# Performance work log

Hardware: AMD Instinct MI355X
Metric: run time of the kernel (lower is better)

Reference implementation:

```python
import jax, jax.numpy as jnp
import numpy as np

B, S, V, E, H = 256, 141, 1000, 256, 512


def setup_inputs() -> dict:
    key = jax.random.key(0)
    ks = jax.random.split(key, 12)
    sd = 0.05
    return {
        "encoder_output": jax.random.normal(ks[0], (B, E), dtype=jnp.float32),
        "target_sequence": jax.random.randint(ks[1], (B, S), 0, V),
        "embedding": jax.random.normal(ks[2], (V, E), dtype=jnp.float32) * sd,
        "W_ih": jax.random.normal(ks[3], (4 * H, 2 * E), dtype=jnp.float32) * sd,
        "W_hh": jax.random.normal(ks[4], (4 * H, H), dtype=jnp.float32) * sd,
        "b_ih": jnp.zeros((4 * H,), dtype=jnp.float32),
        "b_hh": jnp.zeros((4 * H,), dtype=jnp.float32),
        "attn_W": jax.random.normal(ks[5], (H, H + E), dtype=jnp.float32) * sd,
        "attn_b": jnp.zeros((H,), dtype=jnp.float32),
        "v_w": jax.random.normal(ks[6], (H,), dtype=jnp.float32) * sd,
        "out_W": jax.random.normal(ks[7], (V, H), dtype=jnp.float32) * sd,
        "out_b": jnp.zeros((V,), dtype=jnp.float32),
    }


def reference(encoder_output, target_sequence, embedding, W_ih, W_hh, b_ih, b_hh,
              attn_W, attn_b, v_w, out_W, out_b):
    # embedded: [B, S, E] -> scan over time: [S, B, E]
    embedded = embedding[target_sequence]
    xs = jnp.swapaxes(embedded, 0, 1)

    h0 = jnp.zeros((B, H), dtype=encoder_output.dtype)
    c0 = jnp.zeros((B, H), dtype=encoder_output.dtype)

    def step(carry, x_t):
        h, c = carry  # [B, H]
        # Bahdanau attention over src_len=1 (encoder_output.unsqueeze(1))
        cat = jnp.concatenate([h, encoder_output], axis=-1)      # [B, H+E]
        energy = jnp.tanh(cat @ attn_W.T + attn_b)               # [B, H]
        score = energy @ v_w                                      # [B]
        # softmax over a single source position -> weight 1
        w = jax.nn.softmax(score[:, None], axis=1)               # [B, 1]
        context = w * encoder_output                              # [B, E]
        lstm_in = jnp.concatenate([x_t, context], axis=-1)       # [B, 2E]
        gates = lstm_in @ W_ih.T + b_ih + h @ W_hh.T + b_hh      # [B, 4H]
        i, f, g, o = jnp.split(gates, 4, axis=-1)                # torch gate order
        i = jax.nn.sigmoid(i)
        f = jax.nn.sigmoid(f)
        g = jnp.tanh(g)
        o = jax.nn.sigmoid(o)
        c_new = f * c + i * g
        h_new = o * jnp.tanh(c_new)
        return (h_new, c_new), h_new

    _, hs = jax.lax.scan(step, (h0, c0), xs)                     # hs: [S, B, H]
    logits = jnp.einsum('sbh,vh->bsv', hs, out_W) + out_b        # [B, S, V]
    return logits
```

## Files before the change

kernel.cpp:

```cpp
#include <hip/hip_runtime.h>

typedef __attribute__((ext_vector_type(8))) short bf16x8;
typedef __attribute__((ext_vector_type(4))) float f32x4;
typedef __attribute__((ext_vector_type(4))) unsigned short u16x4;

#define Bdim 256
#define Sdim 141
#define Vdim 1000
#define Edim 256
#define Hdim 512
#define G4H  2048

__device__ __forceinline__ float bf2f(unsigned short u) {
    union { unsigned int i; float f; } x; x.i = ((unsigned int)u) << 16; return x.f;
}
__device__ __forceinline__ unsigned short f2bf(float f) {
    union { float f; unsigned int i; } x; x.f = f;
    unsigned int i = x.i;
    return (unsigned short)((i + 0x7FFFu + ((i >> 16) & 1u)) >> 16);
}
__device__ __forceinline__ float sigmoid_f(float x) { return 1.f / (1.f + __expf(-x)); }
__device__ __forceinline__ float tanh_f(float x)    { return 1.f - 2.f / (__expf(2.f * x) + 1.f); }

__device__ __forceinline__ bf16x8 cvt8(const float* p) {
    const float4 v0 = ((const float4*)p)[0];
    const float4 v1 = ((const float4*)p)[1];
    bf16x8 r;
    r[0] = (short)f2bf(v0.x); r[1] = (short)f2bf(v0.y);
    r[2] = (short)f2bf(v0.z); r[3] = (short)f2bf(v0.w);
    r[4] = (short)f2bf(v1.x); r[5] = (short)f2bf(v1.y);
    r[6] = (short)f2bf(v1.z); r[7] = (short)f2bf(v1.w);
    return r;
}

__global__ __launch_bounds__(256) void f32_to_bf16_4(
    const float4* __restrict__ src, u16x4* __restrict__ dst, int n4)
{
    const int i = blockIdx.x * 256 + threadIdx.x;
    if (i < n4) {
        const float4 v = src[i];
        u16x4 r;
        r[0] = f2bf(v.x); r[1] = f2bf(v.y); r[2] = f2bf(v.z); r[3] = f2bf(v.w);
        dst[i] = r;
    }
}

template <bool BF16OUT>
__global__ __launch_bounds__(256) void gemm_bt_f32in(
    const float* __restrict__ A, int lda, int M,
    const float* __restrict__ Bw, int ldb,
    void* __restrict__ Cv, int ldc,
    const float* __restrict__ bias0,
    const float* __restrict__ bias1,
    int K)
{
    const int m0 = blockIdx.x * 128;
    const int n0 = blockIdx.y * 64;
    const int w    = threadIdx.x >> 6;
    const int l    = threadIdx.x & 63;
    const int lr   = l & 15;
    const int quad = l >> 4;

    int ra0 = m0 + w * 32 + lr;
    int ra1 = ra0 + 16;
    ra0 = ra0 < M ? ra0 : M - 1;
    ra1 = ra1 < M ? ra1 : M - 1;
    const float* pa0 = A + (size_t)ra0 * lda + quad * 8;
    const float* pa1 = A + (size_t)ra1 * lda + quad * 8;
    const float* pb[4];
#pragma unroll
    for (int nj = 0; nj < 4; ++nj)
        pb[nj] = Bw + (size_t)(n0 + nj * 16 + lr) * ldb + quad * 8;

    f32x4 acc[2][4];
#pragma unroll
    for (int mi = 0; mi < 2; ++mi)
#pragma unroll
        for (int nj = 0; nj < 4; ++nj)
            acc[mi][nj] = (f32x4){0.f, 0.f, 0.f, 0.f};

    for (int k = 0; k < K; k += 32) {
        bf16x8 a0 = cvt8(pa0 + k);
        bf16x8 a1 = cvt8(pa1 + k);
#pragma unroll
        for (int nj = 0; nj < 4; ++nj) {
            bf16x8 bb = cvt8(pb[nj] + k);
            acc[0][nj] = __builtin_amdgcn_mfma_f32_16x16x32_bf16(a0, bb, acc[0][nj], 0, 0, 0);
            acc[1][nj] = __builtin_amdgcn_mfma_f32_16x16x32_bf16(a1, bb, acc[1][nj], 0, 0, 0);
        }
    }

#pragma unroll
    for (int nj = 0; nj < 4; ++nj) {
        const int col = n0 + nj * 16 + lr;
        float bv = 0.f;
        if (bias0) bv += bias0[col];
        if (bias1) bv += bias1[col];
#pragma unroll
        for (int mi = 0; mi < 2; ++mi) {
            const int row = m0 + w * 32 + mi * 16 + quad * 4;
#pragma unroll
            for (int r = 0; r < 4; ++r) {
                if (row + r < M) {
                    const float v = acc[mi][nj][r] + bv;
                    if (BF16OUT)
                        ((unsigned short*)Cv)[(size_t)(row + r) * ldc + col] = f2bf(v);
                    else
                        ((float*)Cv)[(size_t)(row + r) * ldc + col] = v;
                }
            }
        }
    }
}

__device__ __forceinline__ void sync_agent(unsigned* bar, int bi, unsigned target) {
    __syncthreads();
    if (threadIdx.x == 0) {
        unsigned* ctr = bar + 256 + bi * 32;
        const unsigned goal = target * 32u;
        __hip_atomic_fetch_add(ctr, 1u, __ATOMIC_RELAXED, __HIP_MEMORY_SCOPE_AGENT);
        int guard = 0;
        while ((__hip_atomic_fetch_add(ctr, 0x10000u, __ATOMIC_RELAXED,
                                       __HIP_MEMORY_SCOPE_AGENT) & 0xFFFFu) < goal
               && ++guard < (1 << 16))
            __builtin_amdgcn_s_sleep(1);
        __builtin_amdgcn_fence(__ATOMIC_ACQUIRE, "workgroup");
    }
    __syncthreads();
}

__device__ __forceinline__ void sync_fast(unsigned* bar, int bi, unsigned target) {
    __syncthreads();
    if (threadIdx.x == 0) {
        unsigned* ctr = bar + 768 + bi * 32;
        const unsigned goal = target * 32u;
        __hip_atomic_fetch_add(ctr, 1u, __ATOMIC_RELAXED, __HIP_MEMORY_SCOPE_WORKGROUP);
        int guard = 0;
        while ((__hip_atomic_fetch_add(ctr, 0x10000u, __ATOMIC_RELAXED,
                                       __HIP_MEMORY_SCOPE_WORKGROUP) & 0xFFFFu) < goal
               && ++guard < (1 << 16))
            __builtin_amdgcn_s_sleep(1);
        __builtin_amdgcn_fence(__ATOMIC_ACQUIRE, "workgroup");
    }
    __syncthreads();
}

__global__ __launch_bounds__(256) void lstm_scan(
    const unsigned short* __restrict__ Whh,
    const unsigned short* __restrict__ emb_proj,
    const float* __restrict__ enc_proj,
    const int* __restrict__ tgt,
    unsigned short* __restrict__ hs,
    unsigned* __restrict__ bar)
{
    const int blk = blockIdx.x;
    const int bi  = blk & 7;
    const int ht  = blk >> 3;
    const int r0  = bi * 32;
    const int h0  = ht * 16;
    const int tid = threadIdx.x;
    const int nf   = tid >> 6;
    const int l    = tid & 63;
    const int lr   = l & 15;
    const int quad = l >> 4;

    __shared__ unsigned short w_lds[4096 * 8];
    __shared__ float g_lds[32][67];

    for (int u = tid; u < 4096; u += 256) {
        const int ulr = u & 15;
        const int uq  = (u >> 4) & 3;
        const int uk  = (u >> 6) & 15;
        const int ug  = u >> 10;
        *(bf16x8*)&w_lds[u * 8] =
            *(const bf16x8*)(Whh + (size_t)(ug * Hdim + h0 + ulr) * Hdim + uk * 32 + uq * 8);
    }

    int xcc;
    asm volatile("s_getreg_b32 %0, hwreg(HW_REG_XCC_ID)" : "=s"(xcc));
    if (tid == 0) {
        __hip_atomic_fetch_or(bar + 512 + bi * 32, 1u << (xcc & 7),
                              __ATOMIC_RELAXED, __HIP_MEMORY_SCOPE_AGENT);
        asm volatile("s_waitcnt vmcnt(0)" ::: "memory");
    }
    sync_agent(bar, bi, 1u);
    const unsigned fl = __hip_atomic_load(bar + 512 + bi * 32,
                              __ATOMIC_RELAXED, __HIP_MEMORY_SCOPE_AGENT);
    const bool fast = (fl & (fl - 1u)) == 0u;

    const int prow = tid & 31;
    const int phc  = (tid >> 5) * 2;
    const int brow = r0 + prow;

    const int* tokp = tgt + (size_t)brow * Sdim;

    const float* encp = enc_proj + (size_t)brow * G4H + h0 + phc;
    float2 env[4];
#pragma unroll
    for (int g = 0; g < 4; ++g)
        env[g] = *(const float2*)(encp + g * Hdim);

    unsigned epk[4];
    {
        const unsigned short* embp = emb_proj + (size_t)tokp[0] * G4H + h0 + phc;
#pragma unroll
        for (int g = 0; g < 4; ++g)
            epk[g] = *(const unsigned*)(embp + g * Hdim);
    }

    const size_t arow0 = (size_t)(r0 + lr) * Hdim + quad * 8;
    const size_t arow1 = (size_t)(r0 + 16 + lr) * Hdim + quad * 8;
    const unsigned short* wlp = w_lds + (size_t)nf * 1024 * 8;

    float c0 = 0.f, c1 = 0.f;

    for (int t = 0; t < Sdim; ++t) {
        const int tn = tokp[t + 1 < Sdim ? t + 1 : t];
        unsigned epkn[4];
        {
            const unsigned short* embn = emb_proj + (size_t)tn * G4H + h0 + phc;
#pragma unroll
            for (int g = 0; g < 4; ++g)
                epkn[g] = *(const unsigned*)(embn + g * Hdim);
        }

        f32x4 acc0 = (f32x4){0.f, 0.f, 0.f, 0.f};
        f32x4 acc1 = (f32x4){0.f, 0.f, 0.f, 0.f};
        if (t > 0) {
            const unsigned short* hprev = hs + (size_t)(t - 1) * (Bdim * Hdim);
#pragma unroll
            for (int k16 = 0; k16 < 16; ++k16) {
                bf16x8 a0 = *(const bf16x8*)(hprev + arow0 + k16 * 32);
                bf16x8 a1 = *(const bf16x8*)(hprev + arow1 + k16 * 32);
                bf16x8 bb = *(const bf16x8*)&wlp[(k16 * 64 + l) * 8];
                acc0 = __builtin_amdgcn_mfma_f32_16x16x32_bf16(a0, bb, acc0, 0, 0, 0);
                acc1 = __builtin_amdgcn_mfma_f32_16x16x32_bf16(a1, bb, acc1, 0, 0, 0);
            }
        }
#pragma unroll
        for (int r = 0; r < 4; ++r) {
            g_lds[quad * 4 + r][nf * 16 + lr]      = acc0[r];
            g_lds[16 + quad * 4 + r][nf * 16 + lr] = acc1[r];
        }
        __syncthreads();

        unsigned hpack = 0;
#pragma unroll
        for (int e = 0; e < 2; ++e) {
            const int c = phc + e;
            const float iv = g_lds[prow][c]      + bf2f((unsigned short)(epk[0] >> (16 * e))) + (e ? env[0].y : env[0].x);
            const float fv = g_lds[prow][16 + c] + bf2f((unsigned short)(epk[1] >> (16 * e))) + (e ? env[1].y : env[1].x);
            const float gv = g_lds[prow][32 + c] + bf2f((unsigned short)(epk[2] >> (16 * e))) + (e ? env[2].y : env[2].x);
            const float ov = g_lds[prow][48 + c] + bf2f((unsigned short)(epk[3] >> (16 * e))) + (e ? env[3].y : env[3].x);
            float cc = e ? c1 : c0;
            const float cn = sigmoid_f(fv) * cc + sigmoid_f(iv) * tanh_f(gv);
            if (e) c1 = cn; else c0 = cn;
            hpack |= ((unsigned)f2bf(sigmoid_f(ov) * tanh_f(cn))) << (16 * e);
        }
        unsigned* hsp = (unsigned*)(hs + (size_t)t * (Bdim * Hdim) + (size_t)brow * Hdim + h0 + phc);
        if (fast)
            *hsp = hpack;
        else
            __hip_atomic_store(hsp, hpack, __ATOMIC_RELAXED, __HIP_MEMORY_SCOPE_AGENT);

        if (t != Sdim - 1) {
            if (fast) sync_fast(bar, bi, (unsigned)(t + 1));
            else      sync_agent(bar, bi, (unsigned)(t + 2));
        }

#pragma unroll
        for (int g = 0; g < 4; ++g)
            epk[g] = epkn[g];
    }
}

__global__ __launch_bounds__(256) void gemm_logits(
    const unsigned short* __restrict__ A,
    const unsigned short* __restrict__ W,
    const float* __restrict__ bias,
    float* __restrict__ out)
{
    const int m0 = blockIdx.x * 128;
    const int n0 = blockIdx.y * 64;
    const int w    = threadIdx.x >> 6;
    const int l    = threadIdx.x & 63;
    const int lr   = l & 15;
    const int quad = l >> 4;

    const unsigned short* pa0 = A + (size_t)(m0 + w * 32 + lr) * Hdim + quad * 8;
    const unsigned short* pa1 = pa0 + (size_t)16 * Hdim;
    const unsigned short* pb[4];
#pragma unroll
    for (int nj = 0; nj < 4; ++nj) {
        int rb = n0 + nj * 16 + lr;
        rb = rb < Vdim ? rb : Vdim - 1;
        pb[nj] = W + (size_t)rb * Hdim + quad * 8;
    }

    f32x4 acc[2][4];
#pragma unroll
    for (int mi = 0; mi < 2; ++mi)
#pragma unroll
        for (int nj = 0; nj < 4; ++nj)
            acc[mi][nj] = (f32x4){0.f, 0.f, 0.f, 0.f};

    for (int k = 0; k < Hdim; k += 32) {
        bf16x8 a0 = *(const bf16x8*)(pa0 + k);
        bf16x8 a1 = *(const bf16x8*)(pa1 + k);
#pragma unroll
        for (int nj = 0; nj < 4; ++nj) {
            bf16x8 bb = *(const bf16x8*)(pb[nj] + k);
            acc[0][nj] = __builtin_amdgcn_mfma_f32_16x16x32_bf16(a0, bb, acc[0][nj], 0, 0, 0);
            acc[1][nj] = __builtin_amdgcn_mfma_f32_16x16x32_bf16(a1, bb, acc[1][nj], 0, 0, 0);
        }
    }

#pragma unroll
    for (int nj = 0; nj < 4; ++nj) {
        const int col = n0 + nj * 16 + lr;
        if (col >= Vdim) continue;
        const float bv = bias[col];
#pragma unroll
        for (int mi = 0; mi < 2; ++mi) {
            const int rowb = m0 + w * 32 + mi * 16 + quad * 4;
#pragma unroll
            for (int r = 0; r < 4; ++r) {
                const int row = rowb + r;
                const int s = row >> 8;
                const int b = row & 255;
                out[((size_t)b * Sdim + s) * Vdim + col] = acc[mi][nj][r] + bv;
            }
        }
    }
}

extern "C" void kernel_launch(void* const* d_in, const int* in_sizes, int n_in,
                              void* d_out, int out_size, void* d_ws, size_t ws_size,
                              hipStream_t stream) {
    const float* enc   = (const float*)d_in[0];
    const int*   tgt   = (const int*)d_in[1];
    const float* emb   = (const float*)d_in[2];
    const float* W_ih  = (const float*)d_in[3];
    const float* W_hh  = (const float*)d_in[4];
    const float* b_ih  = (const float*)d_in[5];
    const float* b_hh  = (const float*)d_in[6];
    const float* out_W = (const float*)d_in[10];
    const float* out_b = (const float*)d_in[11];
    float* out = (float*)d_out;

    char* ws = (char*)d_ws;
    unsigned short* whh_bf   = (unsigned short*)ws;
    unsigned short* outw_bf  = (unsigned short*)(ws + 2097152);
    unsigned short* emb_proj = (unsigned short*)(ws + 3121152);
    float*          enc_proj = (float*)(ws + 7217152);
    unsigned short* hs       = (unsigned short*)(ws + 9314304);
    unsigned*       bar      = (unsigned*)(ws + 46276608);

    hipMemsetAsync(bar, 0, 4096, stream);

    f32_to_bf16_4<<<dim3((262144 + 255) / 256), 256, 0, stream>>>(
        (const float4*)W_hh, (u16x4*)whh_bf, 262144);
    f32_to_bf16_4<<<dim3((128000 + 255) / 256), 256, 0, stream>>>(
        (const float4*)out_W, (u16x4*)outw_bf, 128000);

    gemm_bt_f32in<true><<<dim3(8, 32), 256, 0, stream>>>(
        emb, Edim, Vdim, W_ih, 2 * Edim, emb_proj, G4H, nullptr, nullptr, Edim);
    gemm_bt_f32in<false><<<dim3(2, 32), 256, 0, stream>>>(
        enc, Edim, Bdim, W_ih + Edim, 2 * Edim, enc_proj, G4H, b_ih, b_hh, Edim);
    lstm_scan<<<dim3(256), 256, 0, stream>>>(whh_bf, emb_proj, enc_proj, tgt, hs, bar);
    gemm_logits<<<dim3(282, 16), 256, 0, stream>>>(hs, outw_bf, out_b, out);
}
```

Before: 1.424 ms.

## Repartition LSTM scan into 16 batch groups of 16 rows with 512-thread blocks

The persistent LSTM scan now splits work into 16 batch groups of 16 rows, each spread over 16 blocks covering 32 hidden units, instead of 8 groups of 32 rows over 32 blocks of 16 hidden units. Blocks grow to 512 threads (8 waves), each wave doing one MFMA chain, so the W_hh slice kept in LDS doubles to 128 KB. Fewer blocks share each barrier, which is meant to cut the per-step grid-sync latency that dominates the sequential scan. The cost is a larger LDS footprint, scalar 16-bit h stores in place of packed pairs, and a changed barrier and flag layout.

```diff
diff --git a/kernel.cpp b/kernel.cpp
--- a/kernel.cpp
+++ b/kernel.cpp
@@ -116,8 +116,8 @@
 __device__ __forceinline__ void sync_agent(unsigned* bar, int bi, unsigned target) {
     __syncthreads();
     if (threadIdx.x == 0) {
-        unsigned* ctr = bar + 256 + bi * 32;
-        const unsigned goal = target * 32u;
+        unsigned* ctr = bar + bi * 32;
+        const unsigned goal = target * 16u;
         __hip_atomic_fetch_add(ctr, 1u, __ATOMIC_RELAXED, __HIP_MEMORY_SCOPE_AGENT);
         int guard = 0;
         while ((__hip_atomic_fetch_add(ctr, 0x10000u, __ATOMIC_RELAXED,
@@ -132,8 +132,8 @@
 __device__ __forceinline__ void sync_fast(unsigned* bar, int bi, unsigned target) {
     __syncthreads();
     if (threadIdx.x == 0) {
-        unsigned* ctr = bar + 768 + bi * 32;
-        const unsigned goal = target * 32u;
+        unsigned* ctr = bar + 512 + bi * 32;
+        const unsigned goal = target * 16u;
         __hip_atomic_fetch_add(ctr, 1u, __ATOMIC_RELAXED, __HIP_MEMORY_SCOPE_WORKGROUP);
         int guard = 0;
         while ((__hip_atomic_fetch_add(ctr, 0x10000u, __ATOMIC_RELAXED,
@@ -145,7 +145,7 @@
     __syncthreads();
 }
 
-__global__ __launch_bounds__(256) void lstm_scan(
+__global__ __launch_bounds__(512) void lstm_scan(
     const unsigned short* __restrict__ Whh,
     const unsigned short* __restrict__ emb_proj,
     const float* __restrict__ enc_proj,
@@ -154,114 +154,104 @@
     unsigned* __restrict__ bar)
 {
     const int blk = blockIdx.x;
-    const int bi  = blk & 7;
-    const int ht  = blk >> 3;
-    const int r0  = bi * 32;
-    const int h0  = ht * 16;
+    const int bi  = (blk & 7) * 2 + ((blk >> 3) & 1);
+    const int ht  = blk >> 4;
+    const int r0  = bi * 16;
+    const int h0  = ht * 32;
     const int tid = threadIdx.x;
-    const int nf   = tid >> 6;
+    const int w    = tid >> 6;
     const int l    = tid & 63;
     const int lr   = l & 15;
     const int quad = l >> 4;
 
-    __shared__ unsigned short w_lds[4096 * 8];
-    __shared__ float g_lds[32][67];
-
-    for (int u = tid; u < 4096; u += 256) {
+    __shared__ unsigned short w_lds[8192 * 8];
+    __shared__ float g_lds[16][132];
+
+    for (int u = tid; u < 8192; u += 512) {
         const int ulr = u & 15;
         const int uq  = (u >> 4) & 3;
         const int uk  = (u >> 6) & 15;
-        const int ug  = u >> 10;
+        const int us  = u >> 10;
+        const int grow = (us >> 1) * Hdim + h0 + (us & 1) * 16 + ulr;
         *(bf16x8*)&w_lds[u * 8] =
-            *(const bf16x8*)(Whh + (size_t)(ug * Hdim + h0 + ulr) * Hdim + uk * 32 + uq * 8);
+            *(const bf16x8*)(Whh + (size_t)grow * Hdim + uk * 32 + uq * 8);
     }
 
     int xcc;
     asm volatile("s_getreg_b32 %0, hwreg(HW_REG_XCC_ID)" : "=s"(xcc));
     if (tid == 0) {
-        __hip_atomic_fetch_or(bar + 512 + bi * 32, 1u << (xcc & 7),
+        __hip_atomic_fetch_or(bar + bi * 32 + 16, 1u << (xcc & 7),
                               __ATOMIC_RELAXED, __HIP_MEMORY_SCOPE_AGENT);
         asm volatile("s_waitcnt vmcnt(0)" ::: "memory");
     }
     sync_agent(bar, bi, 1u);
-    const unsigned fl = __hip_atomic_load(bar + 512 + bi * 32,
+    const unsigned fl = __hip_atomic_load(bar + bi * 32 + 16,
                               __ATOMIC_RELAXED, __HIP_MEMORY_SCOPE_AGENT);
     const bool fast = (fl & (fl - 1u)) == 0u;
 
-    const int prow = tid & 31;
-    const int phc  = (tid >> 5) * 2;
+    const int prow = tid >> 5;
+    const int phc  = tid & 31;
     const int brow = r0 + prow;
 
     const int* tokp = tgt + (size_t)brow * Sdim;
 
     const float* encp = enc_proj + (size_t)brow * G4H + h0 + phc;
-    float2 env[4];
+    float env[4];
 #pragma unroll
     for (int g = 0; g < 4; ++g)
-        env[g] = *(const float2*)(encp + g * Hdim);
-
-    unsigned epk[4];
+        env[g] = encp[g * Hdim];
+
+    unsigned short epk[4];
     {
         const unsigned short* embp = emb_proj + (size_t)tokp[0] * G4H + h0 + phc;
 #pragma unroll
         for (int g = 0; g < 4; ++g)
-            epk[g] = *(const unsigned*)(embp + g * Hdim);
-    }
-
-    const size_t arow0 = (size_t)(r0 + lr) * Hdim + quad * 8;
-    const size_t arow1 = (size_t)(r0 + 16 + lr) * Hdim + quad * 8;
-    const unsigned short* wlp = w_lds + (size_t)nf * 1024 * 8;
-
-    float c0 = 0.f, c1 = 0.f;
+            epk[g] = embp[g * Hdim];
+    }
+
+    const size_t arow = (size_t)(r0 + lr) * Hdim + quad * 8;
+    const unsigned short* wlp = w_lds + (size_t)w * 1024 * 8;
+
+    float c0 = 0.f;
 
     for (int t = 0; t < Sdim; ++t) {
         const int tn = tokp[t + 1 < Sdim ? t + 1 : t];
-        unsigned epkn[4];
+        unsigned short epkn[4];
         {
             const unsigned short* embn = emb_proj + (size_t)tn * G4H + h0 + phc;
 #pragma unroll
             for (int g = 0; g < 4; ++g)
-                epkn[g] = *(const unsigned*)(embn + g * Hdim);
-        }
-
-        f32x4 acc0 = (f32x4){0.f, 0.f, 0.f, 0.f};
-        f32x4 acc1 = (f32x4){0.f, 0.f, 0.f, 0.f};
+                epkn[g] = embn[g * Hdim];
+        }
+
+        f32x4 acc = (f32x4){0.f, 0.f, 0.f, 0.f};
         if (t > 0) {
             const unsigned short* hprev = hs + (size_t)(t - 1) * (Bdim * Hdim);
 #pragma unroll
             for (int k16 = 0; k16 < 16; ++k16) {
-                bf16x8 a0 = *(const bf16x8*)(hprev + arow0 + k16 * 32);
-                bf16x8 a1 = *(const bf16x8*)(hprev + arow1 + k16 * 32);
-                bf16x8 bb = *(const bf16x8*)&wlp[(k16 * 64 + l) * 8];
-                acc0 = __builtin_amdgcn_mfma_f32_16x16x32_bf16(a0, bb, acc0, 0, 0, 0);
-                acc1 = __builtin_amdgcn_mfma_f32_16x16x32_bf16(a1, bb, acc1, 0, 0, 0);
+                bf16x8 a = *(const bf16x8*)(hprev + arow + k16 * 32);
+                bf16x8 b = *(const bf16x8*)&wlp[(k16 * 64 + l) * 8];
+                acc = __builtin_amdgcn_mfma_f32_16x16x32_bf16(a, b, acc, 0, 0, 0);
             }
         }
 #pragma unroll
-        for (int r = 0; r < 4; ++r) {
-            g_lds[quad * 4 + r][nf * 16 + lr]      = acc0[r];
-            g_lds[16 + quad * 4 + r][nf * 16 + lr] = acc1[r];
-        }
+        for (int r = 0; r < 4; ++r)
+            g_lds[quad * 4 + r][w * 16 + lr] = acc[r];
         __syncthreads();
 
-        unsigned hpack = 0;
-#pragma unroll
-        for (int e = 0; e < 2; ++e) {
-            const int c = phc + e;
-            const float iv = g_lds[prow][c]      + bf2f((unsigned short)(epk[0] >> (16 * e))) + (e ? env[0].y : env[0].x);
-            const float fv = g_lds[prow][16 + c] + bf2f((unsigned short)(epk[1] >> (16 * e))) + (e ? env[1].y : env[1].x);
-            const float gv = g_lds[prow][32 + c] + bf2f((unsigned short)(epk[2] >> (16 * e))) + (e ? env[2].y : env[2].x);
-            const float ov = g_lds[prow][48 + c] + bf2f((unsigned short)(epk[3] >> (16 * e))) + (e ? env[3].y : env[3].x);
-            float cc = e ? c1 : c0;
-            const float cn = sigmoid_f(fv) * cc + sigmoid_f(iv) * tanh_f(gv);
-            if (e) c1 = cn; else c0 = cn;
-            hpack |= ((unsigned)f2bf(sigmoid_f(ov) * tanh_f(cn))) << (16 * e);
-        }
-        unsigned* hsp = (unsigned*)(hs + (size_t)t * (Bdim * Hdim) + (size_t)brow * Hdim + h0 + phc);
+        const float iv = g_lds[prow][phc]      + bf2f(epk[0]) + env[0];
+        const float fv = g_lds[prow][32 + phc] + bf2f(epk[1]) + env[1];
+        const float gv = g_lds[prow][64 + phc] + bf2f(epk[2]) + env[2];
+        const float ov = g_lds[prow][96 + phc] + bf2f(epk[3]) + env[3];
+        const float cn = sigmoid_f(fv) * c0 + sigmoid_f(iv) * tanh_f(gv);
+        c0 = cn;
+        const unsigned short hv = f2bf(sigmoid_f(ov) * tanh_f(cn));
+
+        unsigned short* hsp = hs + (size_t)t * (Bdim * Hdim) + (size_t)brow * Hdim + h0 + phc;
         if (fast)
-            *hsp = hpack;
+            *hsp = hv;
         else
-            __hip_atomic_store(hsp, hpack, __ATOMIC_RELAXED, __HIP_MEMORY_SCOPE_AGENT);
+            __hip_atomic_store(hsp, hv, __ATOMIC_RELAXED, __HIP_MEMORY_SCOPE_AGENT);
 
         if (t != Sdim - 1) {
             if (fast) sync_fast(bar, bi, (unsigned)(t + 1));
@@ -367,6 +357,6 @@
         emb, Edim, Vdim, W_ih, 2 * Edim, emb_proj, G4H, nullptr, nullptr, Edim);
     gemm_bt_f32in<false><<<dim3(2, 32), 256, 0, stream>>>(
         enc, Edim, Bdim, W_ih + Edim, 2 * Edim, enc_proj, G4H, b_ih, b_hh, Edim);
-    lstm_scan<<<dim3(256), 256, 0, stream>>>(whh_bf, emb_proj, enc_proj, tgt, hs, bar);
+    lstm_scan<<<dim3(256), 512, 0, stream>>>(whh_bf, emb_proj, enc_proj, tgt, hs, bar);
     gemm_logits<<<dim3(282, 16), 256, 0, stream>>>(hs, outw_bf, out_b, out);
 }
```

Result: faster. 1.154 ms (-18.9%).
